# Kernel tuning notes

Hardware: AMD Instinct MI355X
Metric: run time of the kernel (lower is better)

Reference implementation:

```python
import jax, jax.numpy as jnp
import numpy as np

B, T, C, H = 4, 2048, 1024, 16  # batch, seq, d_model, heads
D = C // H                      # head_dim = 64


def setup_inputs() -> dict:
    key = jax.random.key(0)
    ks = jax.random.split(key, 7)
    s = 1.0 / np.sqrt(C)
    return {
        "q_x": jax.random.normal(ks[0], (B, T, C), jnp.float32),
        "Wq": jax.random.normal(ks[1], (C, C), jnp.float32) * s,
        "bq": jax.random.normal(ks[2], (C,), jnp.float32) * 0.01,
        "Wk": jax.random.normal(ks[3], (C, C), jnp.float32) * s,
        "bk": jax.random.normal(ks[4], (C,), jnp.float32) * 0.01,
        "Wv": jax.random.normal(ks[5], (C, C), jnp.float32) * s,
        "bv": jax.random.normal(ks[6], (C,), jnp.float32) * 0.01,
    }


def reference(q_x, Wq, bq, Wk, bk, Wv, bv):
    # Self-attention path (k_x = v_x = q_x). Torch Linear: y = x @ W.T + b.
    q = q_x @ Wq.T + bq          # [B,T,C]
    k = q_x @ Wk.T + bk
    v = q_x @ Wv.T + bv
    # split heads: (B,T,C) -> (B,H,T,D); matches torch reshape(T,B*H,D) layout
    def heads(x):
        return x.reshape(B, T, H, D).transpose(0, 2, 1, 3)
    qh, kh, vh = heads(q), heads(k), heads(v)
    scale = 1.0 / np.sqrt(D)
    attn = jnp.einsum('bhtd,bhsd->bhts', qh, kh) * scale  # [B,H,T,T]
    attn = jax.nn.softmax(attn, axis=-1)
    x = jnp.einsum('bhts,bhsd->bhtd', attn, vh)           # [B,H,T,D]
    # merge heads back -> (B,T,C); batch_first=True output
    return x.transpose(0, 2, 1, 3).reshape(B, T, C)
```

## Files before the change

### kernel.cpp

```cpp
#include <hip/hip_runtime.h>
#include <hip/hip_bf16.h>
#include <stdint.h>
#include <stddef.h>

#define B_ 4
#define T_ 2048
#define C_ 1024
#define H_ 16
#define D_ 64
#define M_ (B_ * T_)

typedef __bf16 bf16x8 __attribute__((ext_vector_type(8)));
typedef float  f32x4  __attribute__((ext_vector_type(4)));
typedef short  s16x4  __attribute__((ext_vector_type(4)));
typedef unsigned short u16x8 __attribute__((ext_vector_type(8)));
typedef unsigned short u16x4 __attribute__((ext_vector_type(4)));
typedef unsigned int   u32x2 __attribute__((ext_vector_type(2)));

__device__ __forceinline__ unsigned short f2bf(float f) {
    union { float f; unsigned int u; } c; c.f = f;
    unsigned int u = c.u;
    unsigned int r = (u + 0x7fffu + ((u >> 16) & 1u)) >> 16;
    return (unsigned short)r;
}

__device__ __forceinline__ unsigned int pack2bf(float a, float b) {
    unsigned int ua = __builtin_bit_cast(unsigned int, a) + 0x8000u;
    unsigned int ub = __builtin_bit_cast(unsigned int, b) + 0x8000u;
    return __builtin_amdgcn_perm(ub, ua, 0x07060302u);
}

__device__ __forceinline__ bf16x8 ld_bf16x8(const unsigned short* p) {
    u16x8 v = *(const u16x8*)p;
    return __builtin_bit_cast(bf16x8, v);
}

__device__ __forceinline__ void gl_lds16(const unsigned short* g, unsigned short* l) {
    __builtin_amdgcn_global_load_lds(
        (const void __attribute__((address_space(1)))*)g,
        (void __attribute__((address_space(3)))*)l, 16, 0, 0);
}

__device__ __forceinline__ f32x4 mfma16(s16x4 a, s16x4 b, f32x4 c) {
#if __has_builtin(__builtin_amdgcn_mfma_f32_16x16x16bf16_1k)
    return __builtin_amdgcn_mfma_f32_16x16x16bf16_1k(a, b, c, 0, 0, 0);
#else
    asm volatile("v_mfma_f32_16x16x16_bf16 %0, %1, %2, %0"
                 : "+v"(c) : "v"(a), "v"(b));
    return c;
#endif
}

__device__ __forceinline__ f32x4 vmax4(f32x4 a, f32x4 b) {
    f32x4 r;
    r.x = fmaxf(a.x, b.x); r.y = fmaxf(a.y, b.y);
    r.z = fmaxf(a.z, b.z); r.w = fmaxf(a.w, b.w);
    return r;
}

#define X4_ ((int64_t)M_ * C_ / 4)
#define W4_ ((int64_t)C_ * C_ / 4)

__global__ __launch_bounds__(256)
void cvt_bf16(const float* __restrict__ x,
              const float* __restrict__ Wq, const float* __restrict__ Wk,
              const float* __restrict__ Wv,
              unsigned short* __restrict__ xb, unsigned short* __restrict__ wb)
{
    const int64_t i4 = (int64_t)blockIdx.x * blockDim.x + threadIdx.x;
    const float* src; unsigned short* dst; int64_t off;
    if (i4 < X4_) { src = x; dst = xb; off = i4; }
    else {
        int64_t j = i4 - X4_;
        int which = (int)(j / W4_);
        off = j - (int64_t)which * W4_;
        src = (which == 0) ? Wq : (which == 1) ? Wk : Wv;
        dst = wb + (int64_t)which * C_ * C_;
    }
    f32x4 v = *(const f32x4*)(src + off * 4);
    u16x4 o = { f2bf(v.x), f2bf(v.y), f2bf(v.z), f2bf(v.w) };
    *(u16x4*)(dst + off * 4) = o;
}

#define K1_ 0.180336880f

__global__ __launch_bounds__(256)
void qkv_gemm(const unsigned short* __restrict__ xb,
              const unsigned short* __restrict__ wb,
              const float* __restrict__ bq, const float* __restrict__ bk,
              const float* __restrict__ bv,
              unsigned short* __restrict__ qo,
              unsigned short* __restrict__ ko,
              unsigned short* __restrict__ vo)
{
    __shared__ alignas(16) unsigned short As[128 * 64];
    __shared__ alignas(16) unsigned short Bs[128 * 64];

    const int tid   = threadIdx.x;
    const int bm    = blockIdx.x;
    const int bn    = blockIdx.y;
    const int which = bn >> 3;
    const int n_base = (bn & 7) * 128;
    const int nrow   = bn * 128;
    const int m_base = bm * 128;

    const float* bias = (which == 0) ? bq : (which == 1) ? bk : bv;

    const int w = tid >> 6, lane = tid & 63;
    const int wr = w >> 1, wc = w & 1;
    const int ln = lane & 15, quad = lane >> 4;

    const int srow   = lane >> 3;
    const int schunk = (lane & 7) ^ srow;
    const int scu    = schunk * 8;

    const f32x4 fz = {0.f, 0.f, 0.f, 0.f};
    f32x4 acc[4][4];
#pragma unroll
    for (int i = 0; i < 4; ++i)
#pragma unroll
        for (int j = 0; j < 4; ++j) acc[i][j] = fz;

    for (int k0 = 0; k0 < C_; k0 += 64) {
        __syncthreads();
#pragma unroll
        for (int i = 0; i < 4; ++i) {
            const int r = w * 32 + i * 8 + srow;
            gl_lds16(xb + (size_t)(m_base + r) * C_ + k0 + scu, As + (w * 4 + i) * 512);
            gl_lds16(wb + (size_t)(nrow  + r) * C_ + k0 + scu, Bs + (w * 4 + i) * 512);
        }
        __syncthreads();

#pragma unroll
        for (int kk = 0; kk < 2; ++kk) {
            bf16x8 af[4], bfr[4];
#pragma unroll
            for (int mi = 0; mi < 4; ++mi) {
                const int r = wr * 64 + mi * 16 + ln;
                af[mi] = ld_bf16x8(&As[r * 64 + (((kk * 4 + quad) ^ (ln & 7)) * 8)]);
            }
#pragma unroll
            for (int ni = 0; ni < 4; ++ni) {
                const int r = wc * 64 + ni * 16 + ln;
                bfr[ni] = ld_bf16x8(&Bs[r * 64 + (((kk * 4 + quad) ^ (ln & 7)) * 8)]);
            }
#pragma unroll
            for (int mi = 0; mi < 4; ++mi)
#pragma unroll
                for (int ni = 0; ni < 4; ++ni)
                    acc[mi][ni] = __builtin_amdgcn_mfma_f32_16x16x32_bf16(
                        af[mi], bfr[ni], acc[mi][ni], 0, 0, 0);
        }
    }

#pragma unroll
    for (int ni = 0; ni < 4; ++ni) {
        const int n_local = n_base + wc * 64 + ni * 16 + ln;
        const float bv_ = bias[n_local];
        const int h = n_local >> 6, d = n_local & 63;
#pragma unroll
        for (int mi = 0; mi < 4; ++mi) {
            const int m0 = m_base + wr * 64 + mi * 16 + quad * 4;
            const int b  = m0 >> 11;
            const int t0 = m0 & (T_ - 1);
            f32x4 v = acc[mi][ni];
            if (which == 2) {
                const int tb   = t0 & ~127;
                const int w128 = t0 & 127;
                const int kvt  = w128 >> 4;
                const int qd   = (w128 >> 2) & 3;
                const int pos  = (kvt >> 1) * 32 + qd * 8 + (kvt & 1) * 4;
                u16x4 pk = { f2bf(v.x + bv_), f2bf(v.y + bv_),
                             f2bf(v.z + bv_), f2bf(v.w + bv_) };
                *(u16x4*)(&vo[((size_t)(b * H_ + h) * D_ + d) * T_ + tb + pos]) = pk;
            } else if (which == 0) {
                unsigned short* dst =
                    qo + ((size_t)(b * H_ + h) * T_ + t0) * (size_t)D_ + d;
                dst[0 * D_] = f2bf((v.x + bv_) * K1_);
                dst[1 * D_] = f2bf((v.y + bv_) * K1_);
                dst[2 * D_] = f2bf((v.z + bv_) * K1_);
                dst[3 * D_] = f2bf((v.w + bv_) * K1_);
            } else {
                unsigned short* dst =
                    ko + ((size_t)(b * H_ + h) * T_ + t0) * (size_t)D_ + d;
                dst[0 * D_] = f2bf(v.x + bv_);
                dst[1 * D_] = f2bf(v.y + bv_);
                dst[2 * D_] = f2bf(v.z + bv_);
                dst[3 * D_] = f2bf(v.w + bv_);
            }
        }
    }
}

__global__ __launch_bounds__(256)
void flash_attn(const unsigned short* __restrict__ qb,
                const unsigned short* __restrict__ kb,
                const unsigned short* __restrict__ vtb,
                float* __restrict__ out)
{
    __shared__ alignas(16) unsigned char smem[36864];
    unsigned short* Ks = (unsigned short*)smem;
    unsigned short* Vs = (unsigned short*)(smem + 16384);
    float* Os = (float*)smem;

    const int tid = threadIdx.x;
    const int qt  = blockIdx.x;
    const int bh  = blockIdx.y;
    const int b   = bh >> 4, h = bh & 15;

    const int w = tid >> 6, lane = tid & 63;
    const int ln = lane & 15, quad = lane >> 4;

    const unsigned short* Qb = qb  + (size_t)bh * T_ * D_;
    const unsigned short* Kb = kb  + (size_t)bh * T_ * D_;
    const unsigned short* Vb = vtb + (size_t)bh * D_ * T_;

    const int qrow0 = qt * 128 + w * 16 + ln;
    const bf16x8 qA0 = ld_bf16x8(&Qb[(size_t)qrow0 * D_ + quad * 8]);
    const bf16x8 qA1 = ld_bf16x8(&Qb[(size_t)qrow0 * D_ + 32 + quad * 8]);
    const bf16x8 qB0 = ld_bf16x8(&Qb[(size_t)(qrow0 + 64) * D_ + quad * 8]);
    const bf16x8 qB1 = ld_bf16x8(&Qb[(size_t)(qrow0 + 64) * D_ + 32 + quad * 8]);

    const int srow   = lane >> 3;
    const int schunk = (lane & 7) ^ srow;
    const int scu    = schunk * 8;
    const int vrow = lane >> 4;

    const f32x4 fz = {0.f, 0.f, 0.f, 0.f};
    float m2a = -3.0e38f, lia = 0.f;
    float m2b = -3.0e38f, lib = 0.f;
    f32x4 accA[4], accB[4];
#pragma unroll
    for (int dt = 0; dt < 4; ++dt) { accA[dt] = fz; accB[dt] = fz; }

    for (int kv0 = 0; kv0 < T_; kv0 += 128) {
        __syncthreads();
#pragma unroll
        for (int i = 0; i < 4; ++i) {
            const int kr = kv0 + w * 32 + i * 8 + srow;
            gl_lds16(Kb + (size_t)kr * D_ + scu, Ks + (w * 4 + i) * 512);
            const int dr = (w * 4 + i) * 4 + vrow;
            const int vcs = (lane & 15) ^ ((i & 1) * 4 + vrow);
            gl_lds16(Vb + (size_t)dr * T_ + kv0 + vcs * 8, Vs + (w * 4 + i) * 512);
        }
        __syncthreads();

        f32x4 sA[8], sB[8];
#pragma unroll
        for (int kvt = 0; kvt < 8; ++kvt) {
            const int r_ = kvt * 16 + ln;
            bf16x8 kf0 = ld_bf16x8(&Ks[r_ * 64 + ((quad)     ^ (ln & 7)) * 8]);
            bf16x8 kf1 = ld_bf16x8(&Ks[r_ * 64 + ((quad + 4) ^ (ln & 7)) * 8]);
            f32x4 cA = fz, cB = fz;
            cA = __builtin_amdgcn_mfma_f32_16x16x32_bf16(kf0, qA0, cA, 0, 0, 0);
            cB = __builtin_amdgcn_mfma_f32_16x16x32_bf16(kf0, qB0, cB, 0, 0, 0);
            cA = __builtin_amdgcn_mfma_f32_16x16x32_bf16(kf1, qA1, cA, 0, 0, 0);
            cB = __builtin_amdgcn_mfma_f32_16x16x32_bf16(kf1, qB1, cB, 0, 0, 0);
            sA[kvt] = cA; sB[kvt] = cB;
        }

        s16x4 pkA[8], pkB[8];
        float alA, alB;
        {
            f32x4 mm = vmax4(vmax4(vmax4(sA[0], sA[1]), vmax4(sA[2], sA[3])),
                             vmax4(vmax4(sA[4], sA[5]), vmax4(sA[6], sA[7])));
            float mx = fmaxf(fmaxf(mm.x, mm.y), fmaxf(mm.z, mm.w));
            mx = fmaxf(mx, __shfl_xor(mx, 16));
            mx = fmaxf(mx, __shfl_xor(mx, 32));
            const float nm = fmaxf(m2a, mx);
            alA = __builtin_amdgcn_exp2f(m2a - nm);
            m2a = nm;
            f32x4 rsv = fz;
#pragma unroll
            for (int kvt = 0; kvt < 8; ++kvt) {
                f32x4 pv;
                pv.x = __builtin_amdgcn_exp2f(sA[kvt].x - m2a);
                pv.y = __builtin_amdgcn_exp2f(sA[kvt].y - m2a);
                pv.z = __builtin_amdgcn_exp2f(sA[kvt].z - m2a);
                pv.w = __builtin_amdgcn_exp2f(sA[kvt].w - m2a);
                rsv += pv;
                u32x2 pd = { pack2bf(pv.x, pv.y), pack2bf(pv.z, pv.w) };
                pkA[kvt] = __builtin_bit_cast(s16x4, pd);
            }
            float rs = (rsv.x + rsv.y) + (rsv.z + rsv.w);
            rs += __shfl_xor(rs, 16);
            rs += __shfl_xor(rs, 32);
            lia = lia * alA + rs;
        }
        {
            f32x4 mm = vmax4(vmax4(vmax4(sB[0], sB[1]), vmax4(sB[2], sB[3])),
                             vmax4(vmax4(sB[4], sB[5]), vmax4(sB[6], sB[7])));
            float mx = fmaxf(fmaxf(mm.x, mm.y), fmaxf(mm.z, mm.w));
            mx = fmaxf(mx, __shfl_xor(mx, 16));
            mx = fmaxf(mx, __shfl_xor(mx, 32));
            const float nm = fmaxf(m2b, mx);
            alB = __builtin_amdgcn_exp2f(m2b - nm);
            m2b = nm;
            f32x4 rsv = fz;
#pragma unroll
            for (int kvt = 0; kvt < 8; ++kvt) {
                f32x4 pv;
                pv.x = __builtin_amdgcn_exp2f(sB[kvt].x - m2b);
                pv.y = __builtin_amdgcn_exp2f(sB[kvt].y - m2b);
                pv.z = __builtin_amdgcn_exp2f(sB[kvt].z - m2b);
                pv.w = __builtin_amdgcn_exp2f(sB[kvt].w - m2b);
                rsv += pv;
                u32x2 pd = { pack2bf(pv.x, pv.y), pack2bf(pv.z, pv.w) };
                pkB[kvt] = __builtin_bit_cast(s16x4, pd);
            }
            float rs = (rsv.x + rsv.y) + (rsv.z + rsv.w);
            rs += __shfl_xor(rs, 16);
            rs += __shfl_xor(rs, 32);
            lib = lib * alB + rs;
        }

#pragma unroll
        for (int dt = 0; dt < 4; ++dt) { accA[dt] *= alA; accB[dt] *= alB; }

#pragma unroll
        for (int dt = 0; dt < 4; ++dt) {
            const int vr = dt * 16 + ln;
#pragma unroll
            for (int p = 0; p < 4; ++p) {
                const int cl = ((p * 4 + quad) ^ (ln & 7));
                u16x8 vv = *(const u16x8*)(&Vs[vr * 128 + cl * 8]);
                s16x4 v0 = { (short)vv[0], (short)vv[1], (short)vv[2], (short)vv[3] };
                s16x4 v1 = { (short)vv[4], (short)vv[5], (short)vv[6], (short)vv[7] };
                accA[dt] = mfma16(v0, pkA[2 * p],     accA[dt]);
                accB[dt] = mfma16(v0, pkB[2 * p],     accB[dt]);
                accA[dt] = mfma16(v1, pkA[2 * p + 1], accA[dt]);
                accB[dt] = mfma16(v1, pkB[2 * p + 1], accB[dt]);
            }
        }
    }

    __syncthreads();
    const float rva = 1.0f / lia, rvb = 1.0f / lib;
#pragma unroll
    for (int dt = 0; dt < 4; ++dt)
#pragma unroll
        for (int r = 0; r < 4; ++r) {
            Os[(w * 16 + ln) * 72 + dt * 16 + quad * 4 + r]        = accA[dt][r] * rva;
            Os[(64 + w * 16 + ln) * 72 + dt * 16 + quad * 4 + r]   = accB[dt][r] * rvb;
        }
    __syncthreads();

    const int q  = tid >> 1;
    const int c0 = (tid & 1) * 32;
    const float* src = &Os[q * 72 + c0];
    float* dst = &out[((size_t)(b * T_ + qt * 128 + q)) * C_ + h * 64 + c0];
#pragma unroll
    for (int i = 0; i < 8; ++i)
        *(f32x4*)(dst + i * 4) = *(const f32x4*)(src + i * 4);
}

extern "C" void kernel_launch(void* const* d_in, const int* in_sizes, int n_in,
                              void* d_out, int out_size, void* d_ws, size_t ws_size,
                              hipStream_t stream) {
    const float* q_x = (const float*)d_in[0];
    const float* Wq  = (const float*)d_in[1];
    const float* bq  = (const float*)d_in[2];
    const float* Wk  = (const float*)d_in[3];
    const float* bk  = (const float*)d_in[4];
    const float* Wv  = (const float*)d_in[5];
    const float* bv  = (const float*)d_in[6];
    float* out = (float*)d_out;

    const size_t elems = (size_t)M_ * C_;
    unsigned short* xb  = (unsigned short*)d_ws;
    unsigned short* wb  = xb + elems;
    unsigned short* qb  = wb + (size_t)3 * C_ * C_;
    unsigned short* kb  = qb + elems;
    unsigned short* vtb = kb + elems;
    (void)ws_size; (void)in_sizes; (void)n_in; (void)out_size;

    const int64_t total4 = X4_ + 3 * W4_;
    cvt_bf16<<<(int)(total4 / 256), 256, 0, stream>>>(q_x, Wq, Wk, Wv, xb, wb);

    qkv_gemm<<<dim3(M_ / 128, 24), 256, 0, stream>>>(
        xb, wb, bq, bk, bv, qb, kb, vtb);

    flash_attn<<<dim3(T_ / 128, B_ * H_), 256, 0, stream>>>(qb, kb, vtb, out);
}
```

Baseline: 292.8 us.

## Double-buffer K tiles and use 16x16x32 MFMA for PV product

K tiles are now double-buffered in LDS: the next K tile is prefetched while the current one is used for QK^T, and the V load is issued early so it overlaps the softmax, with an extra barrier before the PV stage. The PV product also switches from pairs of 16x16x16 MFMAs to single 16x16x32 MFMAs by packing two probability fragments into one 8-wide operand. This aims to hide global-to-LDS latency and halve the PV MFMA issue count. In exchange LDS use grows from 36 KB to 48 KB, which may lower occupancy, and each iteration now has two barriers.

```diff
diff --git a/kernel.cpp b/kernel.cpp
--- a/kernel.cpp
+++ b/kernel.cpp
@@ -12,10 +12,9 @@
 
 typedef __bf16 bf16x8 __attribute__((ext_vector_type(8)));
 typedef float  f32x4  __attribute__((ext_vector_type(4)));
-typedef short  s16x4  __attribute__((ext_vector_type(4)));
 typedef unsigned short u16x8 __attribute__((ext_vector_type(8)));
 typedef unsigned short u16x4 __attribute__((ext_vector_type(4)));
-typedef unsigned int   u32x2 __attribute__((ext_vector_type(2)));
+typedef unsigned int   u32x4 __attribute__((ext_vector_type(4)));
 
 __device__ __forceinline__ unsigned short f2bf(float f) {
     union { float f; unsigned int u; } c; c.f = f;
@@ -39,16 +38,6 @@
     __builtin_amdgcn_global_load_lds(
         (const void __attribute__((address_space(1)))*)g,
         (void __attribute__((address_space(3)))*)l, 16, 0, 0);
-}
-
-__device__ __forceinline__ f32x4 mfma16(s16x4 a, s16x4 b, f32x4 c) {
-#if __has_builtin(__builtin_amdgcn_mfma_f32_16x16x16bf16_1k)
-    return __builtin_amdgcn_mfma_f32_16x16x16bf16_1k(a, b, c, 0, 0, 0);
-#else
-    asm volatile("v_mfma_f32_16x16x16_bf16 %0, %1, %2, %0"
-                 : "+v"(c) : "v"(a), "v"(b));
-    return c;
-#endif
 }
 
 __device__ __forceinline__ f32x4 vmax4(f32x4 a, f32x4 b) {
@@ -198,10 +187,9 @@
                 const unsigned short* __restrict__ vtb,
                 float* __restrict__ out)
 {
-    __shared__ alignas(16) unsigned char smem[36864];
-    unsigned short* Ks = (unsigned short*)smem;
-    unsigned short* Vs = (unsigned short*)(smem + 16384);
+    __shared__ alignas(16) unsigned char smem[49152];
     float* Os = (float*)smem;
+    unsigned short* Vs = (unsigned short*)(smem + 32768);
 
     const int tid = threadIdx.x;
     const int qt  = blockIdx.x;
@@ -233,17 +221,32 @@
 #pragma unroll
     for (int dt = 0; dt < 4; ++dt) { accA[dt] = fz; accB[dt] = fz; }
 
-    for (int kv0 = 0; kv0 < T_; kv0 += 128) {
-        __syncthreads();
+    auto stageK = [&](int kv0, int buf) {
+        unsigned short* Ks = (unsigned short*)(smem + buf * 16384);
 #pragma unroll
         for (int i = 0; i < 4; ++i) {
             const int kr = kv0 + w * 32 + i * 8 + srow;
             gl_lds16(Kb + (size_t)kr * D_ + scu, Ks + (w * 4 + i) * 512);
+        }
+    };
+    auto stageV = [&](int kv0) {
+#pragma unroll
+        for (int i = 0; i < 4; ++i) {
             const int dr = (w * 4 + i) * 4 + vrow;
             const int vcs = (lane & 15) ^ ((i & 1) * 4 + vrow);
             gl_lds16(Vb + (size_t)dr * T_ + kv0 + vcs * 8, Vs + (w * 4 + i) * 512);
         }
+    };
+
+    stageK(0, 0);
+
+    for (int kv0 = 0; kv0 < T_; kv0 += 128) {
+        const int cur = (kv0 >> 7) & 1;
         __syncthreads();
+        stageV(kv0);
+        if (kv0 + 128 < T_) stageK(kv0 + 128, cur ^ 1);
+
+        const unsigned short* Ks = (const unsigned short*)(smem + cur * 16384);
 
         f32x4 sA[8], sB[8];
 #pragma unroll
@@ -259,7 +262,7 @@
             sA[kvt] = cA; sB[kvt] = cB;
         }
 
-        s16x4 pkA[8], pkB[8];
+        u32x4 pksA[4], pksB[4];
         float alA, alB;
         {
             f32x4 mm = vmax4(vmax4(vmax4(sA[0], sA[1]), vmax4(sA[2], sA[3])),
@@ -272,15 +275,21 @@
             m2a = nm;
             f32x4 rsv = fz;
 #pragma unroll
-            for (int kvt = 0; kvt < 8; ++kvt) {
-                f32x4 pv;
-                pv.x = __builtin_amdgcn_exp2f(sA[kvt].x - m2a);
-                pv.y = __builtin_amdgcn_exp2f(sA[kvt].y - m2a);
-                pv.z = __builtin_amdgcn_exp2f(sA[kvt].z - m2a);
-                pv.w = __builtin_amdgcn_exp2f(sA[kvt].w - m2a);
-                rsv += pv;
-                u32x2 pd = { pack2bf(pv.x, pv.y), pack2bf(pv.z, pv.w) };
-                pkA[kvt] = __builtin_bit_cast(s16x4, pd);
+            for (int p = 0; p < 4; ++p) {
+                f32x4 e0, e1;
+                e0.x = __builtin_amdgcn_exp2f(sA[2*p].x - m2a);
+                e0.y = __builtin_amdgcn_exp2f(sA[2*p].y - m2a);
+                e0.z = __builtin_amdgcn_exp2f(sA[2*p].z - m2a);
+                e0.w = __builtin_amdgcn_exp2f(sA[2*p].w - m2a);
+                e1.x = __builtin_amdgcn_exp2f(sA[2*p+1].x - m2a);
+                e1.y = __builtin_amdgcn_exp2f(sA[2*p+1].y - m2a);
+                e1.z = __builtin_amdgcn_exp2f(sA[2*p+1].z - m2a);
+                e1.w = __builtin_amdgcn_exp2f(sA[2*p+1].w - m2a);
+                rsv += e0; rsv += e1;
+                pksA[p][0] = pack2bf(e0.x, e0.y);
+                pksA[p][1] = pack2bf(e0.z, e0.w);
+                pksA[p][2] = pack2bf(e1.x, e1.y);
+                pksA[p][3] = pack2bf(e1.z, e1.w);
             }
             float rs = (rsv.x + rsv.y) + (rsv.z + rsv.w);
             rs += __shfl_xor(rs, 16);
@@ -298,15 +307,21 @@
             m2b = nm;
             f32x4 rsv = fz;
 #pragma unroll
-            for (int kvt = 0; kvt < 8; ++kvt) {
-                f32x4 pv;
-                pv.x = __builtin_amdgcn_exp2f(sB[kvt].x - m2b);
-                pv.y = __builtin_amdgcn_exp2f(sB[kvt].y - m2b);
-                pv.z = __builtin_amdgcn_exp2f(sB[kvt].z - m2b);
-                pv.w = __builtin_amdgcn_exp2f(sB[kvt].w - m2b);
-                rsv += pv;
-                u32x2 pd = { pack2bf(pv.x, pv.y), pack2bf(pv.z, pv.w) };
-                pkB[kvt] = __builtin_bit_cast(s16x4, pd);
+            for (int p = 0; p < 4; ++p) {
+                f32x4 e0, e1;
+                e0.x = __builtin_amdgcn_exp2f(sB[2*p].x - m2b);
+                e0.y = __builtin_amdgcn_exp2f(sB[2*p].y - m2b);
+                e0.z = __builtin_amdgcn_exp2f(sB[2*p].z - m2b);
+                e0.w = __builtin_amdgcn_exp2f(sB[2*p].w - m2b);
+                e1.x = __builtin_amdgcn_exp2f(sB[2*p+1].x - m2b);
+                e1.y = __builtin_amdgcn_exp2f(sB[2*p+1].y - m2b);
+                e1.z = __builtin_amdgcn_exp2f(sB[2*p+1].z - m2b);
+                e1.w = __builtin_amdgcn_exp2f(sB[2*p+1].w - m2b);
+                rsv += e0; rsv += e1;
+                pksB[p][0] = pack2bf(e0.x, e0.y);
+                pksB[p][1] = pack2bf(e0.z, e0.w);
+                pksB[p][2] = pack2bf(e1.x, e1.y);
+                pksB[p][3] = pack2bf(e1.z, e1.w);
             }
             float rs = (rsv.x + rsv.y) + (rsv.z + rsv.w);
             rs += __shfl_xor(rs, 16);
@@ -317,19 +332,19 @@
 #pragma unroll
         for (int dt = 0; dt < 4; ++dt) { accA[dt] *= alA; accB[dt] *= alB; }
 
+        __syncthreads();
+
 #pragma unroll
         for (int dt = 0; dt < 4; ++dt) {
             const int vr = dt * 16 + ln;
 #pragma unroll
             for (int p = 0; p < 4; ++p) {
                 const int cl = ((p * 4 + quad) ^ (ln & 7));
-                u16x8 vv = *(const u16x8*)(&Vs[vr * 128 + cl * 8]);
-                s16x4 v0 = { (short)vv[0], (short)vv[1], (short)vv[2], (short)vv[3] };
-                s16x4 v1 = { (short)vv[4], (short)vv[5], (short)vv[6], (short)vv[7] };
-                accA[dt] = mfma16(v0, pkA[2 * p],     accA[dt]);
-                accB[dt] = mfma16(v0, pkB[2 * p],     accB[dt]);
-                accA[dt] = mfma16(v1, pkA[2 * p + 1], accA[dt]);
-                accB[dt] = mfma16(v1, pkB[2 * p + 1], accB[dt]);
+                bf16x8 vv = ld_bf16x8(&Vs[vr * 128 + cl * 8]);
+                accA[dt] = __builtin_amdgcn_mfma_f32_16x16x32_bf16(
+                    vv, __builtin_bit_cast(bf16x8, pksA[p]), accA[dt], 0, 0, 0);
+                accB[dt] = __builtin_amdgcn_mfma_f32_16x16x32_bf16(
+                    vv, __builtin_bit_cast(bf16x8, pksB[p]), accB[dt], 0, 0, 0);
             }
         }
     }
```

New measurement: 281.2 us. 4.0% less time.
